# Kernel tuning notes

Measured on AMD Instinct MI355X. Metric: run time of the kernel, lower is better.

## Reference

```python
import jax, jax.numpy as jnp
import numpy as np

D_MODEL = 512
N_HEADS = 8
D_HEAD = D_MODEL // N_HEADS
MAX_LEN = 5000


def _make_pe():
    # sinusoidal table for relative positions -MAX_LEN..+MAX_LEN
    pos = np.arange(-MAX_LEN, MAX_LEN + 1, dtype=np.float32)[:, None]
    div = np.exp(np.arange(0, D_MODEL, 2, dtype=np.float32) * (-np.log(10000.0) / D_MODEL))
    pe = np.zeros((2 * MAX_LEN + 1, D_MODEL), dtype=np.float32)
    pe[:, 0::2] = np.sin(pos * div)
    pe[:, 1::2] = np.cos(pos * div)
    return jnp.asarray(pe)


def setup_inputs() -> dict:
    key = jax.random.key(0)
    ks = jax.random.split(key, 10)
    B, S = 8, 512
    xavier = lambda k: jax.random.uniform(k, (D_MODEL, D_MODEL), jnp.float32,
                                          -np.sqrt(6.0 / (2 * D_MODEL)), np.sqrt(6.0 / (2 * D_MODEL)))
    return {
        "x": jax.random.normal(ks[0], (B, S, D_MODEL), jnp.float32),
        "wq": xavier(ks[1]), "bq": jnp.zeros((D_MODEL,), jnp.float32),
        "wk": xavier(ks[2]), "bk": jnp.zeros((D_MODEL,), jnp.float32),
        "wv": xavier(ks[3]), "bv": jnp.zeros((D_MODEL,), jnp.float32),
        "wo": xavier(ks[4]), "bo": jnp.zeros((D_MODEL,), jnp.float32),
        "wr": xavier(ks[5]),
        "u": jnp.zeros((N_HEADS, D_HEAD), jnp.float32),
        "v_bias": jnp.zeros((N_HEADS, D_HEAD), jnp.float32),
        "pe": _make_pe(),
    }


def reference(x, wq, bq, wk, bk, wv, bv, wo, bo, wr, u, v_bias, pe):
    B, S, D = x.shape
    H, dh = N_HEADS, D_HEAD
    scale = dh ** -0.5

    # projections (torch Linear: x @ W.T + b) -> [B, H, S, dh]
    def proj(w, b):
        return (x @ w.T + b).reshape(B, S, H, dh).transpose(0, 2, 1, 3)
    q = proj(wq, bq)
    k = proj(wk, bk)
    v = proj(wv, bv)

    # relative position encodings: rel[i,j] = pe[clip(j-i) + MAX_LEN]
    pos = jnp.arange(S)
    rel_idx = jnp.clip(pos[None, :] - pos[:, None], -MAX_LEN, MAX_LEN) + MAX_LEN
    rel_pos = pe[rel_idx]                              # [S, S, D]
    rel_proj = (rel_pos @ wr.T).reshape(S, S, H, dh)   # [S, S, H, dh]
    rel_proj = rel_proj.transpose(2, 0, 1, 3)          # [H, S, S, dh]

    content = jnp.einsum('bhid,bhjd->bhij', q + u[None, :, None, :], k)
    position = jnp.einsum('bhid,hijd->bhij', q + v_bias[None, :, None, :], rel_proj)
    attn = jax.nn.softmax((content + position) * scale, axis=-1)

    out = jnp.einsum('bhij,bhjd->bhid', attn, v)       # [B, H, S, dh]
    out = out.transpose(0, 2, 1, 3).reshape(B, S, D)
    return out @ wo.T + bo
```

## Files before the change

### kernel.cpp

```cpp
#include <hip/hip_runtime.h>
#include <math.h>

#define DM 512
#define NH 8
#define DH 64
#define SEQ 512
#define BATCH 8
#define MR 1023
#define PE_OFF 4489

typedef float4 f4;
typedef __attribute__((ext_vector_type(8))) short bf16x8;
typedef __attribute__((ext_vector_type(4))) float f32x4;
typedef __attribute__((ext_vector_type(8))) unsigned short u16x8;
typedef __attribute__((ext_vector_type(4))) unsigned short u16x4;

__device__ __forceinline__ unsigned short f2bf(float f) {
    unsigned x = __float_as_uint(f);
    unsigned r = x + 0x7fffu + ((x >> 16) & 1u);
    return (unsigned short)(r >> 16);
}
__device__ __forceinline__ float bf2f(unsigned short h) {
    return __uint_as_float(((unsigned)h) << 16);
}
__device__ __forceinline__ f32x4 mfma16(bf16x8 a, bf16x8 b, f32x4 c) {
    return __builtin_amdgcn_mfma_f32_16x16x32_bf16(a, b, c, 0, 0, 0);
}

__device__ __forceinline__ void cvt8(const float* __restrict__ src,
                                     unsigned short* __restrict__ hi,
                                     unsigned short* __restrict__ lo, int i) {
    f4 a = *(const f4*)&src[i];
    f4 b = *(const f4*)&src[i + 4];
    float v[8] = {a.x, a.y, a.z, a.w, b.x, b.y, b.z, b.w};
    u16x8 h, l;
#pragma unroll
    for (int j = 0; j < 8; ++j) {
        unsigned short hb = f2bf(v[j]);
        h[j] = hb;
        l[j] = f2bf(v[j] - bf2f(hb));
    }
    *(u16x8*)&hi[i] = h;
    *(u16x8*)&lo[i] = l;
}

__global__ __launch_bounds__(256) void cvt_kernel(const float* __restrict__ src,
    unsigned short* __restrict__ hi, unsigned short* __restrict__ lo, int n)
{
    const int i = (blockIdx.x * 256 + threadIdx.x) * 8;
    if (i >= n) return;
    cvt8(src, hi, lo, i);
}

__global__ __launch_bounds__(256) void cvt_w_kernel(
    const float* __restrict__ w0, const float* __restrict__ w1,
    const float* __restrict__ w2, const float* __restrict__ w3,
    const float* __restrict__ w4, unsigned short* __restrict__ wb)
{
    const float* src = (blockIdx.y == 0) ? w0 : (blockIdx.y == 1) ? w1 :
                       (blockIdx.y == 2) ? w2 : (blockIdx.y == 3) ? w3 : w4;
    unsigned short* hi = wb + (size_t)blockIdx.y * 524288;
    unsigned short* lo = hi + 262144;
    const int i = (blockIdx.x * 256 + threadIdx.x) * 8;
    cvt8(src, hi, lo, i);
}

__device__ __forceinline__ void gemm_core(
    const unsigned short* __restrict__ Ah, const unsigned short* __restrict__ Al,
    const unsigned short* __restrict__ Wh, const unsigned short* __restrict__ Wl,
    int m0, int n0, f32x4 acc[2][2],
    unsigned short* LAh, unsigned short* LAl,
    unsigned short* LBh, unsigned short* LBl)
{
    const int tid = threadIdx.x;
    const int lane = tid & 63, wid = tid >> 6;
    const int wm = (wid >> 1) << 5, wn = (wid & 1) << 5;
    const int sr = tid >> 2, sc = (tid & 3) << 3;
    const int fr = lane & 15, g = lane >> 4;

#pragma unroll
    for (int i = 0; i < 2; ++i)
#pragma unroll
        for (int j = 0; j < 2; ++j)
            acc[i][j] = (f32x4){0.f, 0.f, 0.f, 0.f};

    const size_t arow = (size_t)(m0 + sr) * DM + sc;
    const size_t wrow = (size_t)(n0 + sr) * DM + sc;

    for (int k0 = 0; k0 < DM; k0 += 32) {
        u16x8 va_h = *(const u16x8*)&Ah[arow + k0];
        u16x8 va_l = *(const u16x8*)&Al[arow + k0];
        u16x8 vb_h = *(const u16x8*)&Wh[wrow + k0];
        u16x8 vb_l = *(const u16x8*)&Wl[wrow + k0];
        if (k0) __syncthreads();
        *(u16x8*)&LAh[sr * 40 + sc] = va_h;
        *(u16x8*)&LAl[sr * 40 + sc] = va_l;
        *(u16x8*)&LBh[sr * 40 + sc] = vb_h;
        *(u16x8*)&LBl[sr * 40 + sc] = vb_l;
        __syncthreads();

        bf16x8 a_h[2], a_l[2], b_h[2], b_l[2];
#pragma unroll
        for (int mi = 0; mi < 2; ++mi) {
            a_h[mi] = *(const bf16x8*)&LAh[(wm + (mi << 4) + fr) * 40 + (g << 3)];
            a_l[mi] = *(const bf16x8*)&LAl[(wm + (mi << 4) + fr) * 40 + (g << 3)];
        }
#pragma unroll
        for (int ni = 0; ni < 2; ++ni) {
            b_h[ni] = *(const bf16x8*)&LBh[(wn + (ni << 4) + fr) * 40 + (g << 3)];
            b_l[ni] = *(const bf16x8*)&LBl[(wn + (ni << 4) + fr) * 40 + (g << 3)];
        }
#pragma unroll
        for (int mi = 0; mi < 2; ++mi)
#pragma unroll
            for (int ni = 0; ni < 2; ++ni) {
                acc[mi][ni] = mfma16(a_h[mi], b_h[ni], acc[mi][ni]);
                acc[mi][ni] = mfma16(a_h[mi], b_l[ni], acc[mi][ni]);
                acc[mi][ni] = mfma16(a_l[mi], b_h[ni], acc[mi][ni]);
            }
    }
}

__global__ __launch_bounds__(256) void qkv_kernel(
    const unsigned short* __restrict__ xh, const unsigned short* __restrict__ xl,
    const unsigned short* __restrict__ wb,
    const float* __restrict__ bq, const float* __restrict__ bk,
    const float* __restrict__ bv, const float* __restrict__ u,
    unsigned short* __restrict__ qh, unsigned short* __restrict__ ql,
    unsigned short* __restrict__ kh, unsigned short* __restrict__ kl,
    unsigned short* __restrict__ vth, unsigned short* __restrict__ vtl)
{
    __shared__ unsigned short LAh[64 * 40], LAl[64 * 40], LBh[64 * 40], LBl[64 * 40];
    const int wsel = blockIdx.x >> 3;
    const int n0 = (blockIdx.x & 7) << 6, m0 = blockIdx.y << 6;
    const unsigned short* Wh = wb + (size_t)wsel * 524288;
    const unsigned short* Wl = Wh + 262144;
    f32x4 acc[2][2];
    gemm_core(xh, xl, Wh, Wl, m0, n0, acc, LAh, LAl, LBh, LBl);

    const int tid = threadIdx.x, lane = tid & 63, wid = tid >> 6;
    const int wm = (wid >> 1) << 5, wn = (wid & 1) << 5;
    const int fr = lane & 15, g = lane >> 4;
    const float* bias = (wsel == 0) ? bq : (wsel == 1) ? bk : bv;

    if (wsel < 2) {
        unsigned short* oh = (wsel == 0) ? qh : kh;
        unsigned short* ol = (wsel == 0) ? ql : kl;
#pragma unroll
        for (int ni = 0; ni < 2; ++ni) {
            const int n_g = n0 + wn + (ni << 4) + fr;
            float bvv = bias[n_g] + ((wsel == 0) ? u[n_g] : 0.f);
            const int h = n_g >> 6, d = n_g & 63;
#pragma unroll
            for (int mi = 0; mi < 2; ++mi)
#pragma unroll
                for (int r = 0; r < 4; ++r) {
                    const int m_g = m0 + wm + (mi << 4) + (g << 2) + r;
                    const int b = m_g >> 9, s = m_g & 511;
                    const float val = acc[mi][ni][r] + bvv;
                    const size_t o = ((size_t)(b * NH + h) * SEQ + s) * DH + d;
                    const unsigned short hb = f2bf(val);
                    oh[o] = hb;
                    ol[o] = f2bf(val - bf2f(hb));
                }
        }
    } else {
#pragma unroll
        for (int ni = 0; ni < 2; ++ni) {
            const int n_g = n0 + wn + (ni << 4) + fr;
            const float bvv = bias[n_g];
            const int h = n_g >> 6, d = n_g & 63;
#pragma unroll
            for (int mi = 0; mi < 2; ++mi) {
                const int m_b = m0 + wm + (mi << 4) + (g << 2);
                const int b = m_b >> 9, s = m_b & 511;
                u16x4 hv, lv;
#pragma unroll
                for (int r = 0; r < 4; ++r) {
                    const float val = acc[mi][ni][r] + bvv;
                    hv[r] = f2bf(val);
                    lv[r] = f2bf(val - bf2f(hv[r]));
                }
                const size_t o = ((size_t)(b * NH + h) * DH + d) * SEQ + s;
                *(u16x4*)&vth[o] = hv;
                *(u16x4*)&vtl[o] = lv;
            }
        }
    }
}

__global__ __launch_bounds__(256) void rm_kernel(
    const unsigned short* __restrict__ peh, const unsigned short* __restrict__ pel,
    const unsigned short* __restrict__ wrh, const unsigned short* __restrict__ wrl,
    unsigned short* __restrict__ rmh, unsigned short* __restrict__ rml)
{
    __shared__ unsigned short LAh[64 * 40], LAl[64 * 40], LBh[64 * 40], LBl[64 * 40];
    const int n0 = blockIdx.x << 6, m0 = blockIdx.y << 6;
    f32x4 acc[2][2];
    gemm_core(peh, pel, wrh, wrl, m0, n0, acc, LAh, LAl, LBh, LBl);

    const int tid = threadIdx.x, lane = tid & 63, wid = tid >> 6;
    const int wm = (wid >> 1) << 5, wn = (wid & 1) << 5;
    const int fr = lane & 15, g = lane >> 4;
#pragma unroll
    for (int ni = 0; ni < 2; ++ni) {
        const int n_g = n0 + wn + (ni << 4) + fr;
        const int h = n_g >> 6, d = n_g & 63;
#pragma unroll
        for (int mi = 0; mi < 2; ++mi)
#pragma unroll
            for (int r = 0; r < 4; ++r) {
                const int dd = m0 + wm + (mi << 4) + (g << 2) + r;
                const float val = acc[mi][ni][r];
                const size_t o = (((size_t)h << 10) + dd) * DH + d;
                const unsigned short hb = f2bf(val);
                rmh[o] = hb;
                rml[o] = f2bf(val - bf2f(hb));
            }
    }
}

__global__ __launch_bounds__(256) void out_kernel(
    const unsigned short* __restrict__ cth, const unsigned short* __restrict__ ctl,
    const unsigned short* __restrict__ woh, const unsigned short* __restrict__ wol,
    const float* __restrict__ bo, float* __restrict__ out)
{
    __shared__ unsigned short LAh[64 * 40], LAl[64 * 40], LBh[64 * 40], LBl[64 * 40];
    const int n0 = blockIdx.x << 6, m0 = blockIdx.y << 6;
    f32x4 acc[2][2];
    gemm_core(cth, ctl, woh, wol, m0, n0, acc, LAh, LAl, LBh, LBl);

    const int tid = threadIdx.x, lane = tid & 63, wid = tid >> 6;
    const int wm = (wid >> 1) << 5, wn = (wid & 1) << 5;
    const int fr = lane & 15, g = lane >> 4;
#pragma unroll
    for (int ni = 0; ni < 2; ++ni) {
        const int n_g = n0 + wn + (ni << 4) + fr;
        const float bvv = bo[n_g];
#pragma unroll
        for (int mi = 0; mi < 2; ++mi)
#pragma unroll
            for (int r = 0; r < 4; ++r) {
                const int m_g = m0 + wm + (mi << 4) + (g << 2) + r;
                out[(size_t)m_g * DM + n_g] = acc[mi][ni][r] + bvv;
            }
    }
}

__global__ __launch_bounds__(64) void corr_kernel(
    const unsigned short* __restrict__ rmh, const unsigned short* __restrict__ rml,
    const float* __restrict__ u, const float* __restrict__ vb,
    float* __restrict__ rc)
{
    const int h = blockIdx.y;
    const int dd = (blockIdx.x << 6) + threadIdx.x;
    float s = 0.f;
    if (dd < MR) {
        const size_t ro = (((size_t)h << 10) + dd) * DH;
        const float* uu = u + h * DH;
        const float* vv = vb + h * DH;
        for (int d = 0; d < DH; ++d)
            s = fmaf(vv[d] - uu[d], bf2f(rmh[ro + d]) + bf2f(rml[ro + d]), s);
    }
    rc[((size_t)h << 10) + dd] = s;
}

__global__ __launch_bounds__(256) void attn_kernel(
    const unsigned short* __restrict__ qh_g, const unsigned short* __restrict__ ql_g,
    const unsigned short* __restrict__ kh_g, const unsigned short* __restrict__ kl_g,
    const unsigned short* __restrict__ vh_g, const unsigned short* __restrict__ vl_g,
    const unsigned short* __restrict__ rmh, const unsigned short* __restrict__ rml,
    const float* __restrict__ rc,
    unsigned short* __restrict__ cth, unsigned short* __restrict__ ctl)
{
    __shared__ unsigned short Kh[64][72], Kl[64][72], Vh[64][72], Vl[64][72];
    __shared__ unsigned short Pdd[4][16][84];
    __shared__ float Pt[4][16][68];

    const int tid = threadIdx.x;
    const int lane = tid & 63, wid = tid >> 6;
    const int g = lane >> 4, c = lane & 15;
    const int i0 = blockIdx.x << 6;
    const int h = blockIdx.y, b = blockIdx.z;
    const int R0 = i0 + (wid << 4);
    const size_t bh = (size_t)(b * NH + h) * (SEQ * DH);

    const int srow = tid >> 3;
    const int sch = (tid & 7) << 3;

    bf16x8 qhf[2], qlf[2];
#pragma unroll
    for (int ks = 0; ks < 2; ++ks) {
        const size_t qo = bh + (size_t)(R0 + c) * DH + (ks << 5) + (g << 3);
        qhf[ks] = *(const bf16x8*)&qh_g[qo];
        qlf[ks] = *(const bf16x8*)&ql_g[qo];
    }

    f32x4 Oacc[4];
#pragma unroll
    for (int nf = 0; nf < 4; ++nf) Oacc[nf] = (f32x4){0.f, 0.f, 0.f, 0.f};
    float m_r[4] = {-3e38f, -3e38f, -3e38f, -3e38f};
    float l_r[4] = {0.f, 0.f, 0.f, 0.f};

    const float* rch = rc + (h << 10);
    const unsigned short* rmhh = rmh + ((size_t)h << 16);
    const unsigned short* rmlh = rml + ((size_t)h << 16);

    u16x8 p0, p1, p2, p3, p4, p5, p6, p7;
    {
        const size_t kb = bh + (size_t)srow * DH + sch;
        p0 = *(const u16x8*)&kh_g[kb];
        p1 = *(const u16x8*)&kh_g[kb + 32 * DH];
        p2 = *(const u16x8*)&kl_g[kb];
        p3 = *(const u16x8*)&kl_g[kb + 32 * DH];
        const size_t vb_ = bh + (size_t)srow * SEQ + sch;
        p4 = *(const u16x8*)&vh_g[vb_];
        p5 = *(const u16x8*)&vh_g[vb_ + 32 * SEQ];
        p6 = *(const u16x8*)&vl_g[vb_];
        p7 = *(const u16x8*)&vl_g[vb_ + 32 * SEQ];
    }

    for (int jt = 0; jt < 8; ++jt) {
        const int j0 = jt << 6;
        const int base = j0 - i0 + 448;
        __syncthreads();
        *(u16x8*)&Kh[srow][sch] = p0;
        *(u16x8*)&Kh[srow + 32][sch] = p1;
        *(u16x8*)&Kl[srow][sch] = p2;
        *(u16x8*)&Kl[srow + 32][sch] = p3;
        *(u16x8*)&Vh[srow][sch] = p4;
        *(u16x8*)&Vh[srow + 32][sch] = p5;
        *(u16x8*)&Vl[srow][sch] = p6;
        *(u16x8*)&Vl[srow + 32][sch] = p7;
        __syncthreads();
        if (jt < 7) {
            const int jn = j0 + 64;
            const size_t kb = bh + (size_t)(jn + srow) * DH + sch;
            p0 = *(const u16x8*)&kh_g[kb];
            p1 = *(const u16x8*)&kh_g[kb + 32 * DH];
            p2 = *(const u16x8*)&kl_g[kb];
            p3 = *(const u16x8*)&kl_g[kb + 32 * DH];
            const size_t vb_ = bh + (size_t)srow * SEQ + jn + sch;
            p4 = *(const u16x8*)&vh_g[vb_];
            p5 = *(const u16x8*)&vh_g[vb_ + 32 * SEQ];
            p6 = *(const u16x8*)&vl_g[vb_];
            p7 = *(const u16x8*)&vl_g[vb_ + 32 * SEQ];
        }

        __builtin_amdgcn_s_setprio(1);
        f32x4 accs[4];
#pragma unroll
        for (int nf = 0; nf < 4; ++nf) accs[nf] = (f32x4){0.f, 0.f, 0.f, 0.f};
#pragma unroll
        for (int ks = 0; ks < 2; ++ks)
#pragma unroll
            for (int nf = 0; nf < 4; ++nf) {
                bf16x8 b_h = *(const bf16x8*)&Kh[(nf << 4) + c][(ks << 5) + (g << 3)];
                bf16x8 b_l = *(const bf16x8*)&Kl[(nf << 4) + c][(ks << 5) + (g << 3)];
                accs[nf] = mfma16(qhf[ks], b_h, accs[nf]);
                accs[nf] = mfma16(qhf[ks], b_l, accs[nf]);
                accs[nf] = mfma16(qlf[ks], b_h, accs[nf]);
            }

        const int base_g = j0 - R0 + 496;
#pragma unroll
        for (int f = 0; f < 5; ++f) {
            f32x4 ap = (f32x4){0.f, 0.f, 0.f, 0.f};
#pragma unroll
            for (int ks = 0; ks < 2; ++ks) {
                const size_t ro = (size_t)(base_g + (f << 4) + c) * DH
                                + (ks << 5) + (g << 3);
                bf16x8 b_h = *(const bf16x8*)&rmhh[ro];
                bf16x8 b_l = *(const bf16x8*)&rmlh[ro];
                ap = mfma16(qhf[ks], b_h, ap);
                ap = mfma16(qhf[ks], b_l, ap);
                ap = mfma16(qlf[ks], b_h, ap);
            }
            const float rcv = rch[base_g + (f << 4) + c];
#pragma unroll
            for (int r = 0; r < 4; ++r)
                Pdd[wid][(g << 2) + r][(f << 4) + c] = f2bf(ap[r] + rcv);
        }
        __builtin_amdgcn_s_setprio(0);

#pragma unroll
        for (int r = 0; r < 4; ++r) {
            const int irow = (g << 2) + r;
            float sc[4];
#pragma unroll
            for (int nf = 0; nf < 4; ++nf) {
                const int ddl = (nf << 4) + c - irow + 15;
                sc[nf] = (accs[nf][r] + bf2f(Pdd[wid][irow][ddl])) * 0.125f;
            }
            float mt = fmaxf(fmaxf(sc[0], sc[1]), fmaxf(sc[2], sc[3]));
#pragma unroll
            for (int off = 8; off; off >>= 1) mt = fmaxf(mt, __shfl_xor(mt, off, 16));
            const float mn = fmaxf(m_r[r], mt);
            const float alpha = __expf(m_r[r] - mn);
            m_r[r] = mn;
            float rs = 0.f;
#pragma unroll
            for (int nf = 0; nf < 4; ++nf) {
                const float p = __expf(sc[nf] - mn);
                Pt[wid][irow][(nf << 4) + c] = p;
                rs += p;
            }
#pragma unroll
            for (int off = 8; off; off >>= 1) rs += __shfl_xor(rs, off, 16);
            l_r[r] = l_r[r] * alpha + rs;
#pragma unroll
            for (int nf = 0; nf < 4; ++nf) Oacc[nf][r] *= alpha;
        }

        __builtin_amdgcn_s_setprio(1);
#pragma unroll
        for (int ks = 0; ks < 2; ++ks) {
            f4 pv0 = *(const f4*)&Pt[wid][c][(ks << 5) + (g << 3)];
            f4 pv1 = *(const f4*)&Pt[wid][c][(ks << 5) + (g << 3) + 4];
            float pv[8] = {pv0.x, pv0.y, pv0.z, pv0.w, pv1.x, pv1.y, pv1.z, pv1.w};
            bf16x8 ph, pl;
#pragma unroll
            for (int e = 0; e < 8; ++e) {
                const unsigned short hb = f2bf(pv[e]);
                ph[e] = (short)hb;
                pl[e] = (short)f2bf(pv[e] - bf2f(hb));
            }
#pragma unroll
            for (int nf = 0; nf < 4; ++nf) {
                bf16x8 v_h = *(const bf16x8*)&Vh[(nf << 4) + c][(ks << 5) + (g << 3)];
                bf16x8 v_l = *(const bf16x8*)&Vl[(nf << 4) + c][(ks << 5) + (g << 3)];
                Oacc[nf] = mfma16(ph, v_h, Oacc[nf]);
                Oacc[nf] = mfma16(ph, v_l, Oacc[nf]);
                Oacc[nf] = mfma16(pl, v_h, Oacc[nf]);
            }
        }
        __builtin_amdgcn_s_setprio(0);
    }

    float inv[4];
#pragma unroll
    for (int r = 0; r < 4; ++r) inv[r] = 1.f / l_r[r];
#pragma unroll
    for (int nf = 0; nf < 4; ++nf)
#pragma unroll
        for (int r = 0; r < 4; ++r) {
            const float val = Oacc[nf][r] * inv[r];
            const int s = R0 + (g << 2) + r;
            const int d = (h << 6) + (nf << 4) + c;
            const size_t o = ((size_t)(b * SEQ) + s) * DM + d;
            const unsigned short hb = f2bf(val);
            cth[o] = hb;
            ctl[o] = f2bf(val - bf2f(hb));
        }
}

extern "C" void kernel_launch(void* const* d_in, const int* in_sizes, int n_in,
                              void* d_out, int out_size, void* d_ws, size_t ws_size,
                              hipStream_t stream)
{
    const float* x  = (const float*)d_in[0];
    const float* wq = (const float*)d_in[1];
    const float* bq = (const float*)d_in[2];
    const float* wk = (const float*)d_in[3];
    const float* bk = (const float*)d_in[4];
    const float* wv = (const float*)d_in[5];
    const float* bv = (const float*)d_in[6];
    const float* wo = (const float*)d_in[7];
    const float* bo = (const float*)d_in[8];
    const float* wr = (const float*)d_in[9];
    const float* u  = (const float*)d_in[10];
    const float* vb = (const float*)d_in[11];
    const float* pe = (const float*)d_in[12];
    float* out = (float*)d_out;
    unsigned short* us = (unsigned short*)d_ws;

    unsigned short* xh  = us;
    unsigned short* xl  = us + 2097152;
    unsigned short* wb  = us + 4194304;
    unsigned short* peh = us + 6815744;
    unsigned short* pel = us + 7340032;
    unsigned short* qh  = us + 7864320;
    unsigned short* ql  = us + 9961472;
    unsigned short* kh  = us + 12058624;
    unsigned short* kl  = us + 14155776;
    unsigned short* vth = us + 16252928;
    unsigned short* vtl = us + 18350080;
    unsigned short* rmh = us + 20447232;
    unsigned short* rml = us + 20971520;
    unsigned short* cth = us + 21495808;
    unsigned short* ctl = us + 23592960;
    float* rc = (float*)(us + 25690112);

    unsigned short* woh = wb + 3 * 524288;
    unsigned short* wol = woh + 262144;
    unsigned short* wrh = wb + 4 * 524288;
    unsigned short* wrl = wrh + 262144;

    dim3 blk(256);
    cvt_kernel<<<1024, blk, 0, stream>>>(x, xh, xl, 2097152);
    cvt_w_kernel<<<dim3(128, 5), blk, 0, stream>>>(wq, wk, wv, wo, wr, wb);
    cvt_kernel<<<256, blk, 0, stream>>>(pe + (size_t)PE_OFF * DM, peh, pel, 523776);

    qkv_kernel<<<dim3(24, 64), blk, 0, stream>>>(xh, xl, wb, bq, bk, bv, u,
                                                 qh, ql, kh, kl, vth, vtl);
    rm_kernel<<<dim3(8, 16), blk, 0, stream>>>(peh, pel, wrh, wrl, rmh, rml);
    corr_kernel<<<dim3(16, 8), dim3(64), 0, stream>>>(rmh, rml, u, vb, rc);
    attn_kernel<<<dim3(8, 8, 8), blk, 0, stream>>>(qh, ql, kh, kl, vth, vtl,
                                                   rmh, rml, rc, cth, ctl);
    out_kernel<<<dim3(8, 64), blk, 0, stream>>>(cth, ctl, woh, wol, bo, out);
}
```

Baseline: 127.1 us.

## Merge conversion kernels, enlarge GEMM tiles, fuse correction into rm, drop P low part

The three fp32-to-bf16 split conversion launches become one kernel. The shared GEMM core moves from 64x64 to 128x64 tiles, halving the grid for the qkv, rm and out kernels. The positional-bias correction term is now computed inside rm_kernel from fp32 accumulators, which removes the separate corr_kernel launch and its reread of rm. In attention, probabilities are stored once as bf16 and the P low-part MFMA is dropped, cutting LDS traffic and a third of the PV MFMAs at some cost in accuracy.

```diff
diff --git a/kernel.cpp b/kernel.cpp
--- a/kernel.cpp
+++ b/kernel.cpp
@@ -44,64 +44,72 @@
     *(u16x8*)&lo[i] = l;
 }
 
-__global__ __launch_bounds__(256) void cvt_kernel(const float* __restrict__ src,
-    unsigned short* __restrict__ hi, unsigned short* __restrict__ lo, int n)
-{
-    const int i = (blockIdx.x * 256 + threadIdx.x) * 8;
-    if (i >= n) return;
-    cvt8(src, hi, lo, i);
-}
-
-__global__ __launch_bounds__(256) void cvt_w_kernel(
+__global__ __launch_bounds__(256) void cvt_all_kernel(
+    const float* __restrict__ x,
     const float* __restrict__ w0, const float* __restrict__ w1,
     const float* __restrict__ w2, const float* __restrict__ w3,
-    const float* __restrict__ w4, unsigned short* __restrict__ wb)
-{
-    const float* src = (blockIdx.y == 0) ? w0 : (blockIdx.y == 1) ? w1 :
-                       (blockIdx.y == 2) ? w2 : (blockIdx.y == 3) ? w3 : w4;
-    unsigned short* hi = wb + (size_t)blockIdx.y * 524288;
-    unsigned short* lo = hi + 262144;
-    const int i = (blockIdx.x * 256 + threadIdx.x) * 8;
-    cvt8(src, hi, lo, i);
-}
-
-__device__ __forceinline__ void gemm_core(
+    const float* __restrict__ w4, const float* __restrict__ pe,
+    unsigned short* __restrict__ xh, unsigned short* __restrict__ xl,
+    unsigned short* __restrict__ wb,
+    unsigned short* __restrict__ peh, unsigned short* __restrict__ pel)
+{
+    const int bid = blockIdx.x, tid = threadIdx.x;
+    if (bid < 1024) {
+        cvt8(x, xh, xl, (bid * 256 + tid) * 8);
+    } else if (bid < 1664) {
+        const int wsel = (bid - 1024) >> 7;
+        const float* src = (wsel == 0) ? w0 : (wsel == 1) ? w1 :
+                           (wsel == 2) ? w2 : (wsel == 3) ? w3 : w4;
+        unsigned short* hi = wb + (size_t)wsel * 524288;
+        cvt8(src, hi, hi + 262144, (((bid - 1024) & 127) * 256 + tid) * 8);
+    } else {
+        const int i = ((bid - 1664) * 256 + tid) * 8;
+        if (i < 523776) cvt8(pe, peh, pel, i);
+    }
+}
+
+__device__ __forceinline__ void gemm_core128(
     const unsigned short* __restrict__ Ah, const unsigned short* __restrict__ Al,
     const unsigned short* __restrict__ Wh, const unsigned short* __restrict__ Wl,
-    int m0, int n0, f32x4 acc[2][2],
+    int m0, int n0, f32x4 acc[4][2],
     unsigned short* LAh, unsigned short* LAl,
     unsigned short* LBh, unsigned short* LBl)
 {
     const int tid = threadIdx.x;
     const int lane = tid & 63, wid = tid >> 6;
-    const int wm = (wid >> 1) << 5, wn = (wid & 1) << 5;
-    const int sr = tid >> 2, sc = (tid & 3) << 3;
+    const int wm = (wid >> 1) << 6, wn = (wid & 1) << 5;
+    const int ar = tid >> 1, ac = (tid & 1) << 4;
+    const int br = tid >> 2, bc = (tid & 3) << 3;
     const int fr = lane & 15, g = lane >> 4;
 
 #pragma unroll
-    for (int i = 0; i < 2; ++i)
+    for (int i = 0; i < 4; ++i)
 #pragma unroll
         for (int j = 0; j < 2; ++j)
             acc[i][j] = (f32x4){0.f, 0.f, 0.f, 0.f};
 
-    const size_t arow = (size_t)(m0 + sr) * DM + sc;
-    const size_t wrow = (size_t)(n0 + sr) * DM + sc;
+    const size_t arow = (size_t)(m0 + ar) * DM + ac;
+    const size_t wrow = (size_t)(n0 + br) * DM + bc;
 
     for (int k0 = 0; k0 < DM; k0 += 32) {
-        u16x8 va_h = *(const u16x8*)&Ah[arow + k0];
-        u16x8 va_l = *(const u16x8*)&Al[arow + k0];
-        u16x8 vb_h = *(const u16x8*)&Wh[wrow + k0];
-        u16x8 vb_l = *(const u16x8*)&Wl[wrow + k0];
+        u16x8 a0 = *(const u16x8*)&Ah[arow + k0];
+        u16x8 a1 = *(const u16x8*)&Ah[arow + k0 + 8];
+        u16x8 a2 = *(const u16x8*)&Al[arow + k0];
+        u16x8 a3 = *(const u16x8*)&Al[arow + k0 + 8];
+        u16x8 b0 = *(const u16x8*)&Wh[wrow + k0];
+        u16x8 b1 = *(const u16x8*)&Wl[wrow + k0];
         if (k0) __syncthreads();
-        *(u16x8*)&LAh[sr * 40 + sc] = va_h;
-        *(u16x8*)&LAl[sr * 40 + sc] = va_l;
-        *(u16x8*)&LBh[sr * 40 + sc] = vb_h;
-        *(u16x8*)&LBl[sr * 40 + sc] = vb_l;
+        *(u16x8*)&LAh[ar * 40 + ac] = a0;
+        *(u16x8*)&LAh[ar * 40 + ac + 8] = a1;
+        *(u16x8*)&LAl[ar * 40 + ac] = a2;
+        *(u16x8*)&LAl[ar * 40 + ac + 8] = a3;
+        *(u16x8*)&LBh[br * 40 + bc] = b0;
+        *(u16x8*)&LBl[br * 40 + bc] = b1;
         __syncthreads();
 
-        bf16x8 a_h[2], a_l[2], b_h[2], b_l[2];
-#pragma unroll
-        for (int mi = 0; mi < 2; ++mi) {
+        bf16x8 a_h[4], a_l[4], b_h[2], b_l[2];
+#pragma unroll
+        for (int mi = 0; mi < 4; ++mi) {
             a_h[mi] = *(const bf16x8*)&LAh[(wm + (mi << 4) + fr) * 40 + (g << 3)];
             a_l[mi] = *(const bf16x8*)&LAl[(wm + (mi << 4) + fr) * 40 + (g << 3)];
         }
@@ -111,7 +119,7 @@
             b_l[ni] = *(const bf16x8*)&LBl[(wn + (ni << 4) + fr) * 40 + (g << 3)];
         }
 #pragma unroll
-        for (int mi = 0; mi < 2; ++mi)
+        for (int mi = 0; mi < 4; ++mi)
 #pragma unroll
             for (int ni = 0; ni < 2; ++ni) {
                 acc[mi][ni] = mfma16(a_h[mi], b_h[ni], acc[mi][ni]);
@@ -120,6 +128,10 @@
             }
     }
 }
+
+#define GEMM_LDS \
+    __shared__ unsigned short LAh[128 * 40], LAl[128 * 40]; \
+    __shared__ unsigned short LBh[64 * 40], LBl[64 * 40];
 
 __global__ __launch_bounds__(256) void qkv_kernel(
     const unsigned short* __restrict__ xh, const unsigned short* __restrict__ xl,
@@ -130,16 +142,16 @@
     unsigned short* __restrict__ kh, unsigned short* __restrict__ kl,
     unsigned short* __restrict__ vth, unsigned short* __restrict__ vtl)
 {
-    __shared__ unsigned short LAh[64 * 40], LAl[64 * 40], LBh[64 * 40], LBl[64 * 40];
+    GEMM_LDS
     const int wsel = blockIdx.x >> 3;
-    const int n0 = (blockIdx.x & 7) << 6, m0 = blockIdx.y << 6;
+    const int n0 = (blockIdx.x & 7) << 6, m0 = blockIdx.y << 7;
     const unsigned short* Wh = wb + (size_t)wsel * 524288;
     const unsigned short* Wl = Wh + 262144;
-    f32x4 acc[2][2];
-    gemm_core(xh, xl, Wh, Wl, m0, n0, acc, LAh, LAl, LBh, LBl);
+    f32x4 acc[4][2];
+    gemm_core128(xh, xl, Wh, Wl, m0, n0, acc, LAh, LAl, LBh, LBl);
 
     const int tid = threadIdx.x, lane = tid & 63, wid = tid >> 6;
-    const int wm = (wid >> 1) << 5, wn = (wid & 1) << 5;
+    const int wm = (wid >> 1) << 6, wn = (wid & 1) << 5;
     const int fr = lane & 15, g = lane >> 4;
     const float* bias = (wsel == 0) ? bq : (wsel == 1) ? bk : bv;
 
@@ -152,7 +164,7 @@
             float bvv = bias[n_g] + ((wsel == 0) ? u[n_g] : 0.f);
             const int h = n_g >> 6, d = n_g & 63;
 #pragma unroll
-            for (int mi = 0; mi < 2; ++mi)
+            for (int mi = 0; mi < 4; ++mi)
 #pragma unroll
                 for (int r = 0; r < 4; ++r) {
                     const int m_g = m0 + wm + (mi << 4) + (g << 2) + r;
@@ -171,7 +183,7 @@
             const float bvv = bias[n_g];
             const int h = n_g >> 6, d = n_g & 63;
 #pragma unroll
-            for (int mi = 0; mi < 2; ++mi) {
+            for (int mi = 0; mi < 4; ++mi) {
                 const int m_b = m0 + wm + (mi << 4) + (g << 2);
                 const int b = m_b >> 9, s = m_b & 511;
                 u16x4 hv, lv;
@@ -192,22 +204,38 @@
 __global__ __launch_bounds__(256) void rm_kernel(
     const unsigned short* __restrict__ peh, const unsigned short* __restrict__ pel,
     const unsigned short* __restrict__ wrh, const unsigned short* __restrict__ wrl,
-    unsigned short* __restrict__ rmh, unsigned short* __restrict__ rml)
-{
-    __shared__ unsigned short LAh[64 * 40], LAl[64 * 40], LBh[64 * 40], LBl[64 * 40];
-    const int n0 = blockIdx.x << 6, m0 = blockIdx.y << 6;
-    f32x4 acc[2][2];
-    gemm_core(peh, pel, wrh, wrl, m0, n0, acc, LAh, LAl, LBh, LBl);
+    const float* __restrict__ u, const float* __restrict__ vb,
+    unsigned short* __restrict__ rmh, unsigned short* __restrict__ rml,
+    float* __restrict__ rc)
+{
+    GEMM_LDS
+    const int n0 = blockIdx.x << 6, m0 = blockIdx.y << 7;
+    f32x4 acc[4][2];
+    gemm_core128(peh, pel, wrh, wrl, m0, n0, acc, LAh, LAl, LBh, LBl);
 
     const int tid = threadIdx.x, lane = tid & 63, wid = tid >> 6;
-    const int wm = (wid >> 1) << 5, wn = (wid & 1) << 5;
+    const int wm = (wid >> 1) << 6, wn = (wid & 1) << 5;
     const int fr = lane & 15, g = lane >> 4;
+    const int h = n0 >> 6;
+
+    float part[4][4];
+    float wgt[2];
+#pragma unroll
+    for (int ni = 0; ni < 2; ++ni) {
+        const int d = wn + (ni << 4) + fr;
+        wgt[ni] = vb[(h << 6) + d] - u[(h << 6) + d];
+    }
+#pragma unroll
+    for (int mi = 0; mi < 4; ++mi)
+#pragma unroll
+        for (int r = 0; r < 4; ++r) part[mi][r] = 0.f;
+
 #pragma unroll
     for (int ni = 0; ni < 2; ++ni) {
         const int n_g = n0 + wn + (ni << 4) + fr;
-        const int h = n_g >> 6, d = n_g & 63;
-#pragma unroll
-        for (int mi = 0; mi < 2; ++mi)
+        const int d = n_g & 63;
+#pragma unroll
+        for (int mi = 0; mi < 4; ++mi)
 #pragma unroll
             for (int r = 0; r < 4; ++r) {
                 const int dd = m0 + wm + (mi << 4) + (g << 2) + r;
@@ -216,8 +244,25 @@
                 const unsigned short hb = f2bf(val);
                 rmh[o] = hb;
                 rml[o] = f2bf(val - bf2f(hb));
-            }
-    }
+                part[mi][r] = fmaf(wgt[ni], val, part[mi][r]);
+            }
+    }
+
+    __syncthreads();
+    float* cbuf = (float*)LAh;
+#pragma unroll
+    for (int mi = 0; mi < 4; ++mi)
+#pragma unroll
+        for (int r = 0; r < 4; ++r) {
+            float v = part[mi][r];
+#pragma unroll
+            for (int off = 8; off; off >>= 1) v += __shfl_xor(v, off, 16);
+            if (fr == 0)
+                cbuf[((wid & 1) << 7) + wm + (mi << 4) + (g << 2) + r] = v;
+        }
+    __syncthreads();
+    if (tid < 128)
+        rc[((size_t)h << 10) + m0 + tid] = cbuf[tid] + cbuf[128 + tid];
 }
 
 __global__ __launch_bounds__(256) void out_kernel(
@@ -225,44 +270,26 @@
     const unsigned short* __restrict__ woh, const unsigned short* __restrict__ wol,
     const float* __restrict__ bo, float* __restrict__ out)
 {
-    __shared__ unsigned short LAh[64 * 40], LAl[64 * 40], LBh[64 * 40], LBl[64 * 40];
-    const int n0 = blockIdx.x << 6, m0 = blockIdx.y << 6;
-    f32x4 acc[2][2];
-    gemm_core(cth, ctl, woh, wol, m0, n0, acc, LAh, LAl, LBh, LBl);
+    GEMM_LDS
+    const int n0 = blockIdx.x << 6, m0 = blockIdx.y << 7;
+    f32x4 acc[4][2];
+    gemm_core128(cth, ctl, woh, wol, m0, n0, acc, LAh, LAl, LBh, LBl);
 
     const int tid = threadIdx.x, lane = tid & 63, wid = tid >> 6;
-    const int wm = (wid >> 1) << 5, wn = (wid & 1) << 5;
+    const int wm = (wid >> 1) << 6, wn = (wid & 1) << 5;
     const int fr = lane & 15, g = lane >> 4;
 #pragma unroll
     for (int ni = 0; ni < 2; ++ni) {
         const int n_g = n0 + wn + (ni << 4) + fr;
         const float bvv = bo[n_g];
 #pragma unroll
-        for (int mi = 0; mi < 2; ++mi)
+        for (int mi = 0; mi < 4; ++mi)
 #pragma unroll
             for (int r = 0; r < 4; ++r) {
                 const int m_g = m0 + wm + (mi << 4) + (g << 2) + r;
                 out[(size_t)m_g * DM + n_g] = acc[mi][ni][r] + bvv;
             }
     }
-}
-
-__global__ __launch_bounds__(64) void corr_kernel(
-    const unsigned short* __restrict__ rmh, const unsigned short* __restrict__ rml,
-    const float* __restrict__ u, const float* __restrict__ vb,
-    float* __restrict__ rc)
-{
-    const int h = blockIdx.y;
-    const int dd = (blockIdx.x << 6) + threadIdx.x;
-    float s = 0.f;
-    if (dd < MR) {
-        const size_t ro = (((size_t)h << 10) + dd) * DH;
-        const float* uu = u + h * DH;
-        const float* vv = vb + h * DH;
-        for (int d = 0; d < DH; ++d)
-            s = fmaf(vv[d] - uu[d], bf2f(rmh[ro + d]) + bf2f(rml[ro + d]), s);
-    }
-    rc[((size_t)h << 10) + dd] = s;
 }
 
 __global__ __launch_bounds__(256) void attn_kernel(
@@ -275,7 +302,7 @@
 {
     __shared__ unsigned short Kh[64][72], Kl[64][72], Vh[64][72], Vl[64][72];
     __shared__ unsigned short Pdd[4][16][84];
-    __shared__ float Pt[4][16][68];
+    __shared__ unsigned short Pth[4][16][72];
 
     const int tid = threadIdx.x;
     const int lane = tid & 63, wid = tid >> 6;
@@ -322,7 +349,6 @@
 
     for (int jt = 0; jt < 8; ++jt) {
         const int j0 = jt << 6;
-        const int base = j0 - i0 + 448;
         __syncthreads();
         *(u16x8*)&Kh[srow][sch] = p0;
         *(u16x8*)&Kh[srow + 32][sch] = p1;
@@ -402,7 +428,7 @@
 #pragma unroll
             for (int nf = 0; nf < 4; ++nf) {
                 const float p = __expf(sc[nf] - mn);
-                Pt[wid][irow][(nf << 4) + c] = p;
+                Pth[wid][irow][(nf << 4) + c] = f2bf(p);
                 rs += p;
             }
 #pragma unroll
@@ -415,23 +441,13 @@
         __builtin_amdgcn_s_setprio(1);
 #pragma unroll
         for (int ks = 0; ks < 2; ++ks) {
-            f4 pv0 = *(const f4*)&Pt[wid][c][(ks << 5) + (g << 3)];
-            f4 pv1 = *(const f4*)&Pt[wid][c][(ks << 5) + (g << 3) + 4];
-            float pv[8] = {pv0.x, pv0.y, pv0.z, pv0.w, pv1.x, pv1.y, pv1.z, pv1.w};
-            bf16x8 ph, pl;
-#pragma unroll
-            for (int e = 0; e < 8; ++e) {
-                const unsigned short hb = f2bf(pv[e]);
-                ph[e] = (short)hb;
-                pl[e] = (short)f2bf(pv[e] - bf2f(hb));
-            }
+            bf16x8 ph = *(const bf16x8*)&Pth[wid][c][(ks << 5) + (g << 3)];
 #pragma unroll
             for (int nf = 0; nf < 4; ++nf) {
                 bf16x8 v_h = *(const bf16x8*)&Vh[(nf << 4) + c][(ks << 5) + (g << 3)];
                 bf16x8 v_l = *(const bf16x8*)&Vl[(nf << 4) + c][(ks << 5) + (g << 3)];
                 Oacc[nf] = mfma16(ph, v_h, Oacc[nf]);
                 Oacc[nf] = mfma16(ph, v_l, Oacc[nf]);
-                Oacc[nf] = mfma16(pl, v_h, Oacc[nf]);
             }
         }
         __builtin_amdgcn_s_setprio(0);
@@ -497,15 +513,14 @@
     unsigned short* wrl = wrh + 262144;
 
     dim3 blk(256);
-    cvt_kernel<<<1024, blk, 0, stream>>>(x, xh, xl, 2097152);
-    cvt_w_kernel<<<dim3(128, 5), blk, 0, stream>>>(wq, wk, wv, wo, wr, wb);
-    cvt_kernel<<<256, blk, 0, stream>>>(pe + (size_t)PE_OFF * DM, peh, pel, 523776);
-
-    qkv_kernel<<<dim3(24, 64), blk, 0, stream>>>(xh, xl, wb, bq, bk, bv, u,
+    cvt_all_kernel<<<1920, blk, 0, stream>>>(x, wq, wk, wv, wo, wr,
+                                             pe + (size_t)PE_OFF * DM,
+                                             xh, xl, wb, peh, pel);
+    qkv_kernel<<<dim3(24, 32), blk, 0, stream>>>(xh, xl, wb, bq, bk, bv, u,
                                                  qh, ql, kh, kl, vth, vtl);
-    rm_kernel<<<dim3(8, 16), blk, 0, stream>>>(peh, pel, wrh, wrl, rmh, rml);
-    corr_kernel<<<dim3(16, 8), dim3(64), 0, stream>>>(rmh, rml, u, vb, rc);
+    rm_kernel<<<dim3(8, 8), blk, 0, stream>>>(peh, pel, wrh, wrl, u, vb,
+                                              rmh, rml, rc);
     attn_kernel<<<dim3(8, 8, 8), blk, 0, stream>>>(qh, ql, kh, kl, vth, vtl,
                                                    rmh, rml, rc, cth, ctl);
-    out_kernel<<<dim3(8, 64), blk, 0, stream>>>(cth, ctl, woh, wol, bo, out);
-}
+    out_kernel<<<dim3(8, 32), blk, 0, stream>>>(cth, ctl, woh, wol, bo, out);
+}
```

Result: no change. 127.6 us (+0.4%).
